# Performance work log

Measured on AMD Instinct MI355X. Metric: run time of the kernel, lower is better.

Reference implementation:

```python
import jax, jax.numpy as jnp
import numpy as np

DIM = 384; HEADS = 6; POINTS = 4; LEVELS = 3; HID = 96
B = 2; D0 = 12; H0 = 12; W0 = 12
NMID = D0 * H0 * W0          # mid-level tokens
NTOK = 73 * NMID // 8        # total tokens across 3 scales


def _ln(x, w, b, eps=1e-6):
    m = x.mean(-1, keepdims=True)
    v = ((x - m) ** 2).mean(-1, keepdims=True)
    return (x - m) * jax.lax.rsqrt(v + eps) * w + b


def _make_ref(shapes):
    # matches get_reference_points: per-level normalized centers, stacked as (d, x, y)
    refs = []
    for (D_, H_, W_) in shapes:
        d = (jnp.arange(D_, dtype=jnp.float32) + 0.5) / D_
        y = (jnp.arange(H_, dtype=jnp.float32) + 0.5) / H_
        x = (jnp.arange(W_, dtype=jnp.float32) + 0.5) / W_
        dd, yy, xx = jnp.meshgrid(d, y, x, indexing='ij')
        refs.append(jnp.stack([dd.ravel(), xx.ravel(), yy.ravel()], -1))
    return jnp.concatenate(refs, 0)[None, :, None, :]  # [1, N, 1, 3]


def _sample_level(v, D_, H_, W_, loc):
    # v: [B,S,h,hd]; loc: [B,Nq,h,P,3] normalized (d,x,y); trilinear, zero padding,
    # align_corners=False semantics (pixel = norm*size - 0.5)
    Bq, Nq, h, P, _ = loc.shape
    hd = v.shape[-1]
    pd = loc[..., 0] * D_ - 0.5
    px = loc[..., 1] * W_ - 0.5
    py = loc[..., 2] * H_ - 0.5
    d0 = jnp.floor(pd); x0 = jnp.floor(px); y0 = jnp.floor(py)
    fd = pd - d0; fx = px - x0; fy = py - y0
    d0 = d0.astype(jnp.int32); x0 = x0.astype(jnp.int32); y0 = y0.astype(jnp.int32)
    acc = jnp.zeros((Bq, Nq, h, P, hd), v.dtype)
    for dd in (0, 1):  # fixed 8-corner loop
        for dy in (0, 1):
            for dx in (0, 1):
                di = d0 + dd; yi = y0 + dy; xi = x0 + dx
                wgt = (fd if dd else 1.0 - fd) * (fy if dy else 1.0 - fy) * (fx if dx else 1.0 - fx)
                valid = ((di >= 0) & (di < D_) & (yi >= 0) & (yi < H_) & (xi >= 0) & (xi < W_)).astype(v.dtype)
                idx = (jnp.clip(di, 0, D_ - 1) * H_ + jnp.clip(yi, 0, H_ - 1)) * W_ + jnp.clip(xi, 0, W_ - 1)
                idx_t = idx.transpose(0, 1, 3, 2).reshape(Bq, Nq * P, h)
                g = jnp.take_along_axis(v, idx_t[..., None], axis=1)  # [B,Nq*P,h,hd]
                g = g.reshape(Bq, Nq, P, h, hd).transpose(0, 1, 3, 2, 4)
                acc = acc + (wgt * valid)[..., None] * g
    return acc  # [B,Nq,h,P,hd]


def _msdeform(q, ref, feat, shapes, off_w, off_b, aw_w, aw_b, val_w, val_b, out_w, out_b):
    Bq, Nq, C = q.shape
    hd = C // HEADS
    value = (feat @ val_w + val_b).reshape(Bq, -1, HEADS, hd)
    off = (q @ off_w + off_b).reshape(Bq, Nq, HEADS, LEVELS, POINTS, 3)
    aw = jax.nn.softmax((q @ aw_w + aw_b).reshape(Bq, Nq, HEADS, LEVELS * POINTS), -1)
    aw = aw.reshape(Bq, Nq, HEADS, LEVELS, POINTS)
    # offset normalizer in (d, x, y) order -> (D, W, H)
    norm = jnp.array([[D_, W_, H_] for (D_, H_, W_) in shapes], dtype=q.dtype)
    loc = ref[:, :, None, :, None, :] + off / norm[None, None, None, :, None, :]
    out = jnp.zeros((Bq, Nq, HEADS, hd), q.dtype)
    start = 0
    for l, (D_, H_, W_) in enumerate(shapes):
        S = D_ * H_ * W_
        sampled = _sample_level(value[:, start:start + S], D_, H_, W_, loc[:, :, :, l])
        out = out + jnp.einsum('bqhp,bqhpd->bqhd', aw[:, :, :, l], sampled)
        start += S
    return out.reshape(Bq, Nq, C) @ out_w + out_b


def _dwconv_seg(x, Dv, Hv, Wv, w, b):
    Bq, S, C = x.shape
    xv = x.reshape(Bq, Dv, Hv, Wv, C)
    y = jax.lax.conv_general_dilated(xv, w, (1, 1, 1), 'SAME',
                                     dimension_numbers=('NDHWC', 'DHWIO', 'NDHWC'),
                                     feature_group_count=C) + b
    return y.reshape(Bq, S, C)


def _conv_ffn(x, D, H, W, fc1_w, fc1_b, dw_w, dw_b, fc2_w, fc2_b):
    x = x @ fc1_w + fc1_b
    n = x.shape[1] // 73
    x1 = _dwconv_seg(x[:, :64 * n], 2 * D, 2 * H, 2 * W, dw_w, dw_b)
    x2 = _dwconv_seg(x[:, 64 * n:72 * n], D, H, W, dw_w, dw_b)
    x3 = _dwconv_seg(x[:, 72 * n:], D // 2, H // 2, W // 2, dw_w, dw_b)
    x = jax.nn.gelu(jnp.concatenate([x1, x2, x3], 1), approximate=False)
    return x @ fc2_w + fc2_b


def _forward(query, feat, D, H, W,
             qnorm_w, qnorm_b, fnorm_w, fnorm_b, ext_qnorm_w, ext_qnorm_b,
             ext_fnorm_w, ext_fnorm_b, ffn_norm_w, ffn_norm_b,
             off_w, off_b, aw_w, aw_b, val_w, val_b, out_w, out_b,
             fc1_w, fc1_b, dw_w, dw_b, fc2_w, fc2_b):
    n_mid = D * H * W
    n_high = 8 * n_mid
    x2 = query[:, n_high:n_high + n_mid] + feat
    q = jnp.concatenate([query[:, :n_high], x2, query[:, n_high + n_mid:]], 1)
    shapes = [(2 * D, 2 * H, 2 * W), (D, H, W), (D // 2, H // 2, W // 2)]
    ref = _make_ref(shapes)
    qn = _ln(q, qnorm_w, qnorm_b)      # CTI_toC.query_norm
    fn = _ln(q, fnorm_w, fnorm_b)      # CTI_toC.feat_norm
    aq = _ln(qn, ext_qnorm_w, ext_qnorm_b)  # MultiscaleExtractor.query_norm
    af = _ln(fn, ext_fnorm_w, ext_fnorm_b)  # MultiscaleExtractor.feat_norm
    out = qn + _msdeform(aq, ref, af, shapes, off_w, off_b, aw_w, aw_b, val_w, val_b, out_w, out_b)
    out = out + _conv_ffn(_ln(out, ffn_norm_w, ffn_norm_b), D, H, W,
                          fc1_w, fc1_b, dw_w, dw_b, fc2_w, fc2_b)
    return out


def setup_inputs() -> dict:
    key = jax.random.key(0)
    ks = jax.random.split(key, 16)
    w = lambda k, *s: jax.random.normal(k, s, jnp.float32) * 0.02
    NO = HEADS * LEVELS * POINTS * 3
    NA = HEADS * LEVELS * POINTS
    return {
        'query': jax.random.normal(ks[0], (B, NTOK, DIM), jnp.float32),
        'reference_points': jax.random.uniform(ks[1], (1, NTOK, 1, 3), dtype=jnp.float32),
        'feat': jax.random.normal(ks[2], (B, NMID, DIM), jnp.float32),
        'spatial_shapes': jnp.array([[2 * D0, 2 * H0, 2 * W0], [D0, H0, W0], [D0 // 2, H0 // 2, W0 // 2]], jnp.int32),
        'level_start_index': jnp.array([0, 8 * NMID, 9 * NMID], jnp.int32),
        'D': D0, 'H': H0, 'W': W0,
        'qnorm_w': jnp.ones(DIM), 'qnorm_b': jnp.zeros(DIM),
        'fnorm_w': jnp.ones(DIM), 'fnorm_b': jnp.zeros(DIM),
        'ext_qnorm_w': jnp.ones(DIM), 'ext_qnorm_b': jnp.zeros(DIM),
        'ext_fnorm_w': jnp.ones(DIM), 'ext_fnorm_b': jnp.zeros(DIM),
        'ffn_norm_w': jnp.ones(DIM), 'ffn_norm_b': jnp.zeros(DIM),
        'off_w': w(ks[3], DIM, NO), 'off_b': jnp.zeros(NO),
        'aw_w': w(ks[4], DIM, NA), 'aw_b': jnp.zeros(NA),
        'val_w': w(ks[5], DIM, DIM), 'val_b': jnp.zeros(DIM),
        'out_w': w(ks[6], DIM, DIM), 'out_b': jnp.zeros(DIM),
        'fc1_w': w(ks[7], DIM, HID), 'fc1_b': jnp.zeros(HID),
        'dw_w': w(ks[8], 3, 3, 3, 1, HID), 'dw_b': jnp.zeros(HID),
        'fc2_w': w(ks[9], HID, DIM), 'fc2_b': jnp.zeros(DIM),
    }


def reference(query, reference_points, feat, spatial_shapes, level_start_index, D, H, W,
              qnorm_w, qnorm_b, fnorm_w, fnorm_b, ext_qnorm_w, ext_qnorm_b,
              ext_fnorm_w, ext_fnorm_b, ffn_norm_w, ffn_norm_b,
              off_w, off_b, aw_w, aw_b, val_w, val_b, out_w, out_b,
              fc1_w, fc1_b, dw_w, dw_b, fc2_w, fc2_b):
    # reference_points / spatial_shapes / level_start_index are required by the torch
    # signature but unused: CTI_toC recomputes deform inputs internally.
    return _forward(query, feat, D, H, W,
                    qnorm_w, qnorm_b, fnorm_w, fnorm_b, ext_qnorm_w, ext_qnorm_b,
                    ext_fnorm_w, ext_fnorm_b, ffn_norm_w, ffn_norm_b,
                    off_w, off_b, aw_w, aw_b, val_w, val_b, out_w, out_b,
                    fc1_w, fc1_b, dw_w, dw_b, fc2_w, fc2_b)
```

## Files before the change

### kernel.cpp

```cpp
#include <hip/hip_runtime.h>
#include <hip/hip_fp16.h>
#include <cstdint>
#include <cstddef>

#define DIM    384
#define HEADS  6
#define HD     64
#define NTOK   15768
#define NMID   1728
#define BATCH  2
#define ROWS   (BATCH*NTOK)
#define MPAD   31616
#define L1START 13824
#define L2START 15552
#define HID    96
#define VROWS  (ROWS + 8)
#define VSLAB  ((size_t)VROWS * 64)

typedef __attribute__((ext_vector_type(8))) short short8;
typedef __attribute__((ext_vector_type(4))) float floatx4;

__device__ __forceinline__ unsigned short f2bf(float x){
  unsigned u = __float_as_uint(x);
  unsigned r = (u + 0x7FFFu + ((u >> 16) & 1u)) >> 16;
  return (unsigned short)r;
}

__device__ __forceinline__ unsigned cvt_pk_bf16(float lo, float hi){
  unsigned r;
  asm("v_cvt_pk_bf16_f32 %0, %1, %2" : "=v"(r) : "v"(lo), "v"(hi));
  return r;
}

__device__ __forceinline__ float wave_sum(float v){
  #pragma unroll
  for (int o = 32; o; o >>= 1) v += __shfl_xor(v, o, 64);
  return v;
}

__device__ __forceinline__ void ln384(const float* x, float* y,
                                      const float* __restrict__ w,
                                      const float* __restrict__ b, int lane){
  float s = 0.f;
  #pragma unroll
  for (int j = 0; j < 6; j++) s += x[j];
  s = wave_sum(s);
  float m = s * (1.f/384.f);
  float v = 0.f;
  #pragma unroll
  for (int j = 0; j < 6; j++){ float d = x[j] - m; v += d*d; }
  v = wave_sum(v) * (1.f/384.f);
  float rs = rsqrtf(v + 1e-6f);
  #pragma unroll
  for (int j = 0; j < 6; j++){
    int c = j*64 + lane;
    y[j] = (x[j] - m) * rs * w[c] + b[c];
  }
}

__global__ void k_ln_front(const float* __restrict__ query, const float* __restrict__ feat,
                           const float* __restrict__ qw,  const float* __restrict__ qb,
                           const float* __restrict__ fw,  const float* __restrict__ fb,
                           const float* __restrict__ eqw, const float* __restrict__ eqb,
                           const float* __restrict__ efw, const float* __restrict__ efb,
                           float* __restrict__ qn, unsigned short* __restrict__ aq,
                           unsigned short* __restrict__ af){
  int wid = blockIdx.x * (blockDim.x >> 6) + (threadIdx.x >> 6);
  if (wid >= ROWS) return;
  int lane = threadIdx.x & 63;
  int b = wid / NTOK, t = wid - b*NTOK;
  const float* qp = query + (size_t)wid * DIM;
  float x[6];
  #pragma unroll
  for (int j = 0; j < 6; j++) x[j] = qp[j*64 + lane];
  if (t >= L1START && t < L2START){
    const float* fp = feat + ((size_t)b*NMID + (t - L1START)) * DIM;
    #pragma unroll
    for (int j = 0; j < 6; j++) x[j] += fp[j*64 + lane];
  }
  float y[6], z[6];
  ln384(x, y, qw, qb, lane);
  {
    float* o = qn + (size_t)wid * DIM;
    #pragma unroll
    for (int j = 0; j < 6; j++) o[j*64 + lane] = y[j];
  }
  ln384(y, z, eqw, eqb, lane);
  {
    unsigned short* o = aq + (size_t)wid * DIM;
    #pragma unroll
    for (int j = 0; j < 6; j++) o[j*64 + lane] = f2bf(z[j]);
  }
  ln384(x, y, fw, fb, lane);
  ln384(y, z, efw, efb, lane);
  {
    unsigned short* o = af + (size_t)wid * DIM;
    #pragma unroll
    for (int j = 0; j < 6; j++) o[j*64 + lane] = f2bf(z[j]);
  }
}

__global__ void k_ln(const float* __restrict__ in, const float* __restrict__ w,
                     const float* __restrict__ b, unsigned short* __restrict__ out){
  int wid = blockIdx.x * (blockDim.x >> 6) + (threadIdx.x >> 6);
  if (wid >= ROWS) return;
  int lane = threadIdx.x & 63;
  float x[6], y[6];
  const float* p = in + (size_t)wid * DIM;
  #pragma unroll
  for (int j = 0; j < 6; j++) x[j] = p[j*64 + lane];
  ln384(x, y, w, b, lane);
  unsigned short* o = out + (size_t)wid * DIM;
  #pragma unroll
  for (int j = 0; j < 6; j++) o[j*64 + lane] = f2bf(y[j]);
}

__global__ void k_cvt_all(const float* __restrict__ val_w, const float* __restrict__ off_w,
                          const float* __restrict__ aw_w,  const float* __restrict__ out_w,
                          const float* __restrict__ fc1_w, const float* __restrict__ fc2_w,
                          const float* __restrict__ off_b, const float* __restrict__ aw_b,
                          unsigned short* __restrict__ wt_val, unsigned short* __restrict__ wt_offaw,
                          unsigned short* __restrict__ wt_out, unsigned short* __restrict__ wt_fc1,
                          unsigned short* __restrict__ wt_fc2, float* __restrict__ offaw_b,
                          unsigned short* __restrict__ vt_pad){
  int id = blockIdx.x * blockDim.x + threadIdx.x;
  if (id < 147456){
    int n = id / 384, k = id - n*384;
    wt_val[id] = f2bf(val_w[(size_t)k*384 + n]);
  } else if (id < 294912){
    int i = id - 147456;
    int n = i / 384, k = i - n*384;
    float v = 0.f;
    if (n < 216) v = off_w[(size_t)k*216 + n];
    else if (n >= 256 && n < 328) v = aw_w[(size_t)k*72 + (n-256)];
    wt_offaw[i] = f2bf(v);
  } else if (id < 442368){
    int i = id - 294912;
    int n = i / 384, k = i - n*384;
    wt_out[i] = f2bf(out_w[(size_t)k*384 + n]);
  } else if (id < 491520){
    int i = id - 442368;
    int n = i / 384, k = i - n*384;
    wt_fc1[i] = f2bf((n < 96) ? fc1_w[(size_t)k*96 + n] : 0.f);
  } else if (id < 528384){
    int i = id - 491520;
    int n = i / 96, k = i - n*96;
    wt_fc2[i] = f2bf(fc2_w[(size_t)k*384 + n]);
  } else if (id < 528768){
    int n = id - 528384;
    float v = 0.f;
    if (n < 216) v = off_b[n];
    else if (n >= 256 && n < 328) v = aw_b[n-256];
    offaw_b[n] = v;
  } else if (id < 531840){
    int i = id - 528768;
    int hh = i >> 9, rem = i & 511;
    vt_pad[(size_t)hh * VSLAB + (size_t)ROWS * 64 + rem] = 0;
  }
}

template<int OUTMODE>
__global__ __launch_bounds__(256) void k_gemm(
    const unsigned short* __restrict__ A,
    const unsigned short* __restrict__ Wt,
    const float* __restrict__ bias,
    const float* __restrict__ R,
    void* __restrict__ Cv,
    int M, int N, int K){
  __shared__ __align__(16) unsigned short As[128*32];
  __shared__ __align__(16) unsigned short Bs[128*32];
  int tid = threadIdx.x;
  int w = tid >> 6, lane = tid & 63;
  int m0 = blockIdx.y * 128, n0 = blockIdx.x * 128;
  int m_off = (w & 1) * 64, n_off = (w >> 1) * 64;

  floatx4 acc[4][4] = {};

  int sr = lane >> 2;
  int sc = (lane & 3) * 8;
  int lrow = lane & 15;
  int kq = (lane >> 4) * 8;

  for (int k0 = 0; k0 < K; k0 += 32){
    #pragma unroll
    for (int s = 0; s < 2; s++){
      int c = w * 2 + s;
      const unsigned short* ga = A  + (size_t)(m0 + c*16 + sr) * K + k0 + sc;
      __builtin_amdgcn_global_load_lds(
          (const __attribute__((address_space(1))) void*)ga,
          (__attribute__((address_space(3))) void*)(As + c*512), 16, 0, 0);
      const unsigned short* gb = Wt + (size_t)(n0 + c*16 + sr) * K + k0 + sc;
      __builtin_amdgcn_global_load_lds(
          (const __attribute__((address_space(1))) void*)gb,
          (__attribute__((address_space(3))) void*)(Bs + c*512), 16, 0, 0);
    }
    __syncthreads();
    short8 afr[4], bfr[4];
    #pragma unroll
    for (int i = 0; i < 4; i++)
      afr[i] = *(const short8*)(As + (m_off + i*16 + lrow)*32 + kq);
    #pragma unroll
    for (int j = 0; j < 4; j++)
      bfr[j] = *(const short8*)(Bs + (n_off + j*16 + lrow)*32 + kq);
    #pragma unroll
    for (int i = 0; i < 4; i++)
      #pragma unroll
      for (int j = 0; j < 4; j++)
        acc[i][j] = __builtin_amdgcn_mfma_f32_16x16x32_bf16(afr[i], bfr[j], acc[i][j], 0, 0, 0);
    __syncthreads();
  }

  int cn = n0 + n_off + lrow;
  int rbase = m0 + m_off + (lane >> 4) * 4;
  #pragma unroll
  for (int j = 0; j < 4; j++){
    int n = cn + j*16;
    if (n >= N) continue;
    float bj = bias[n];
    #pragma unroll
    for (int i = 0; i < 4; i++){
      int mb = rbase + i*16;
      #pragma unroll
      for (int r = 0; r < 4; r++){
        int m = mb + r;
        if (m < M){
          float v = acc[i][j][r] + bj;
          if (R) v += R[(size_t)m * N + n];
          if (OUTMODE == 0)      ((float*)Cv)[(size_t)m * N + n] = v;
          else if (OUTMODE == 1) ((unsigned short*)Cv)[(size_t)m * N + n] = f2bf(v);
          else {
            ((__half*)Cv)[(size_t)(n >> 6) * VSLAB + (size_t)m * 64 + (n & 63)] =
                __float2half_rn(v);
          }
        }
      }
    }
  }
}

__global__ __launch_bounds__(64, 4) void k_msdeform(const __half* __restrict__ vt,
                                                    const float* __restrict__ offaw,
                                                    unsigned short* __restrict__ msout){
  int head = blockIdx.x;
  int r    = blockIdx.y;
  int lane = threadIdx.x & 63;
  int b = (r >= NTOK) ? 1 : 0;
  int t = r - b * NTOK;

  float refd, refy, refx;
  if (t < L1START){
    int i = t;
    int dd = i / 576; int rem = i - dd*576; int yy = rem / 24; int xx = rem - yy*24;
    refd = (dd + 0.5f) * (1.f/24.f); refy = (yy + 0.5f) * (1.f/24.f); refx = (xx + 0.5f) * (1.f/24.f);
  } else if (t < L2START){
    int i = t - L1START;
    int dd = i / 144; int rem = i - dd*144; int yy = rem / 12; int xx = rem - yy*12;
    refd = (dd + 0.5f) * (1.f/12.f); refy = (yy + 0.5f) * (1.f/12.f); refx = (xx + 0.5f) * (1.f/12.f);
  } else {
    int i = t - L2START;
    int dd = i / 36; int rem = i - dd*36; int yy = rem / 6; int xx = rem - yy*6;
    refd = (dd + 0.5f) * (1.f/6.f); refy = (yy + 0.5f) * (1.f/6.f); refx = (xx + 0.5f) * (1.f/6.f);
  }

  int s   = lane & 15;
  int grp = lane >> 4;

  float logit = (s < 12) ? offaw[(size_t)r * 384 + 256 + head * 12 + s] : -1e30f;
  float mx = logit;
  mx = fmaxf(mx, __shfl_xor(mx, 1, 64));
  mx = fmaxf(mx, __shfl_xor(mx, 2, 64));
  mx = fmaxf(mx, __shfl_xor(mx, 4, 64));
  mx = fmaxf(mx, __shfl_xor(mx, 8, 64));
  float e = (s < 12) ? __expf(logit - mx) : 0.f;
  float sum = e;
  sum += __shfl_xor(sum, 1, 64);
  sum += __shfl_xor(sum, 2, 64);
  sum += __shfl_xor(sum, 4, 64);
  sum += __shfl_xor(sum, 8, 64);
  float aww = e / sum;

  int rowk = 0, wgtk = 0;
  if (s < 12){
    int j = s;
    int l = j >> 2;
    int Dl  = (l == 0) ? 24 : ((l == 1) ? 12 : 6);
    int lst = (l == 0) ? 0  : ((l == 1) ? L1START : L2START);
    const float* op = offaw + (size_t)r * 384 + head * 36 + j * 3;
    float od = op[0], ox = op[1], oy = op[2];
    float fDl = (float)Dl;
    float pd = refd * fDl + od - 0.5f;
    float px = refx * fDl + ox - 0.5f;
    float py = refy * fDl + oy - 0.5f;
    float fld = floorf(pd), flx = floorf(px), fly = floorf(py);
    float fd = pd - fld, fx = px - flx, fy = py - fly;
    int d0 = (int)fld, x0 = (int)flx, y0 = (int)fly;
    int cz = grp >> 1, cy = grp & 1;
    int di = d0 + cz, yi = y0 + cy;
    bool vzy = (di >= 0) & (di < Dl) & (yi >= 0) & (yi < Dl);
    float wz = cz ? fd : 1.f - fd;
    float wy = cy ? fy : 1.f - fy;
    float wp = vzy ? (wz * aww) * wy : 0.f;
    int rs = min(max(x0, 0), Dl - 1);
    float wlo_x = (rs == x0) ? (1.f - fx) : ((rs == x0 + 1) ? fx : 0.f);
    float whi_x = ((rs == x0) && (x0 + 1 < Dl)) ? fx : 0.f;
    int dc = min(max(di, 0), Dl - 1);
    int yc = min(max(yi, 0), Dl - 1);
    rowk = (b * NTOK + lst) + (dc * Dl + yc) * Dl + rs;
    __half2 wh = __floats2half2_rn(wp * wlo_x, wp * whi_x);
    wgtk = *(int*)&wh;
  }

  const char* vbase = (const char*)(vt + (size_t)head * VSLAB);
  unsigned laneoff = (unsigned)(lane & 15) << 4;
  unsigned selperm = (lane & 8) ? 0x03020302u : 0x01000100u;

  uint4 vd[12]; unsigned wv[12];
  #define MS_LOAD(J) { int rw_ = __builtin_amdgcn_ds_swizzle(rowk, ((J) << 5) | 16); \
    vd[J] = *(const uint4*)(vbase + ((((unsigned)rw_) << 7) + laneoff)); }
  MS_LOAD(0)  MS_LOAD(1)  MS_LOAD(2)  MS_LOAD(3)
  MS_LOAD(4)  MS_LOAD(5)  MS_LOAD(6)  MS_LOAD(7)
  MS_LOAD(8)  MS_LOAD(9)  MS_LOAD(10) MS_LOAD(11)
  #undef MS_LOAD
  #define MS_W(J) { unsigned wj_ = (unsigned)__builtin_amdgcn_ds_swizzle(wgtk, ((J) << 5) | 16); \
    wv[J] = __builtin_amdgcn_perm(wj_, wj_, selperm); }
  MS_W(0)  MS_W(1)  MS_W(2)  MS_W(3)
  MS_W(4)  MS_W(5)  MS_W(6)  MS_W(7)
  MS_W(8)  MS_W(9)  MS_W(10) MS_W(11)
  #undef MS_W

  __half2 hz; *(int*)&hz = 0;
  __half2 a0 = hz, a1 = hz, a2 = hz, a3 = hz;
  #pragma unroll
  for (int j = 0; j < 12; j++){
    __half2 wh = *(__half2*)&wv[j];
    uint4 v = vd[j];
    a0 = __hfma2(wh, *(__half2*)&v.x, a0);
    a1 = __hfma2(wh, *(__half2*)&v.y, a1);
    a2 = __hfma2(wh, *(__half2*)&v.z, a2);
    a3 = __hfma2(wh, *(__half2*)&v.w, a3);
  }

  int i0 = *(int*)&a0, i1 = *(int*)&a1, i2 = *(int*)&a2, i3 = *(int*)&a3;
  int p0 = __shfl_xor(i0, 8, 64); int p1 = __shfl_xor(i1, 8, 64);
  int p2 = __shfl_xor(i2, 8, 64); int p3 = __shfl_xor(i3, 8, 64);
  a0 = __hadd2(a0, *(__half2*)&p0);
  a1 = __hadd2(a1, *(__half2*)&p1);
  a2 = __hadd2(a2, *(__half2*)&p2);
  a3 = __hadd2(a3, *(__half2*)&p3);
  float2 f0 = __half22float2(a0), f1 = __half22float2(a1);
  float2 f2 = __half22float2(a2), f3 = __half22float2(a3);
  float sv[8] = {f0.x, f0.y, f1.x, f1.y, f2.x, f2.y, f3.x, f3.y};
  #pragma unroll
  for (int k = 0; k < 8; k++){
    sv[k] += __shfl_xor(sv[k], 16, 64);
    sv[k] += __shfl_xor(sv[k], 32, 64);
  }

  if (lane < 8){
    uint4 pk;
    pk.x = cvt_pk_bf16(sv[0], sv[1]);
    pk.y = cvt_pk_bf16(sv[2], sv[3]);
    pk.z = cvt_pk_bf16(sv[4], sv[5]);
    pk.w = cvt_pk_bf16(sv[6], sv[7]);
    *(uint4*)(msout + (size_t)r * DIM + head * 64 + lane * 8) = pk;
  }
}

__global__ void k_dwconv_gelu(const float* __restrict__ h, const float* __restrict__ dww,
                              const float* __restrict__ dwb, unsigned short* __restrict__ h2){
  int gid = blockIdx.x * blockDim.x + threadIdx.x;
  if (gid >= ROWS * 24) return;
  int c4 = gid % 24;
  int r = gid / 24;
  int c = c4 * 4;
  int b = (r >= NTOK) ? 1 : 0;
  int t = r - b * NTOK;
  int base, DL, i;
  if (t < L1START){ base = 0; DL = 24; i = t; }
  else if (t < L2START){ base = L1START; DL = 12; i = t - L1START; }
  else { base = L2START; DL = 6; i = t - L2START; }
  int dd, yy, xx;
  if (DL == 24){ dd = i / 576; int rem = i - dd*576; yy = rem / 24; xx = rem - yy*24; }
  else if (DL == 12){ dd = i / 144; int rem = i - dd*144; yy = rem / 12; xx = rem - yy*12; }
  else { dd = i / 36; int rem = i - dd*36; yy = rem / 6; xx = rem - yy*6; }
  float4 acc = {0.f, 0.f, 0.f, 0.f};
  #pragma unroll
  for (int kz = 0; kz < 3; kz++){
    int nd = dd + kz - 1; if (nd < 0 || nd >= DL) continue;
    #pragma unroll
    for (int ky = 0; ky < 3; ky++){
      int ny = yy + ky - 1; if (ny < 0 || ny >= DL) continue;
      #pragma unroll
      for (int kx = 0; kx < 3; kx++){
        int nx = xx + kx - 1; if (nx < 0 || nx >= DL) continue;
        int nt = base + (nd * DL + ny) * DL + nx;
        float4 hv = *(const float4*)(h + ((size_t)(b*NTOK + nt)) * HID + c);
        float4 wv = *(const float4*)(dww + (size_t)((kz*3 + ky)*3 + kx) * HID + c);
        acc.x += hv.x * wv.x; acc.y += hv.y * wv.y;
        acc.z += hv.z * wv.z; acc.w += hv.w * wv.w;
      }
    }
  }
  float4 bv = *(const float4*)(dwb + c);
  acc.x += bv.x; acc.y += bv.y; acc.z += bv.z; acc.w += bv.w;
  const float k = 0.70710678118654752440f;
  float g0 = 0.5f * acc.x * (1.f + erff(acc.x * k));
  float g1 = 0.5f * acc.y * (1.f + erff(acc.y * k));
  float g2 = 0.5f * acc.z * (1.f + erff(acc.z * k));
  float g3 = 0.5f * acc.w * (1.f + erff(acc.w * k));
  uint2 pk;
  pk.x = ((unsigned)f2bf(g1) << 16) | (unsigned)f2bf(g0);
  pk.y = ((unsigned)f2bf(g3) << 16) | (unsigned)f2bf(g2);
  *(uint2*)(h2 + (size_t)r * HID + c) = pk;
}

extern "C" void kernel_launch(void* const* d_in, const int* in_sizes, int n_in,
                              void* d_out, int out_size, void* d_ws, size_t ws_size,
                              hipStream_t stream){
  const float* query = (const float*)d_in[0];
  const float* feat  = (const float*)d_in[2];
  const float* qnw = (const float*)d_in[8],  *qnb = (const float*)d_in[9];
  const float* fnw = (const float*)d_in[10], *fnb = (const float*)d_in[11];
  const float* eqw = (const float*)d_in[12], *eqb = (const float*)d_in[13];
  const float* efw = (const float*)d_in[14], *efb = (const float*)d_in[15];
  const float* ffw = (const float*)d_in[16], *ffb = (const float*)d_in[17];
  const float* off_w = (const float*)d_in[18], *off_b = (const float*)d_in[19];
  const float* aw_w  = (const float*)d_in[20], *aw_b  = (const float*)d_in[21];
  const float* val_w = (const float*)d_in[22], *val_b = (const float*)d_in[23];
  const float* out_w = (const float*)d_in[24], *out_b = (const float*)d_in[25];
  const float* fc1_w = (const float*)d_in[26], *fc1_b = (const float*)d_in[27];
  const float* dw_w  = (const float*)d_in[28], *dw_b  = (const float*)d_in[29];
  const float* fc2_w = (const float*)d_in[30], *fc2_b = (const float*)d_in[31];
  float* out = (float*)d_out;

  char* p = (char*)d_ws;
  float* qn             = (float*)p;          p += (size_t)ROWS*384*4;
  unsigned short* aq    = (unsigned short*)p; p += (size_t)MPAD*384*2;
  unsigned short* af    = (unsigned short*)p; p += (size_t)MPAD*384*2;
  __half* value_t       = (__half*)p;         p += (size_t)HEADS*VSLAB*2;
  float* offaw          = (float*)p;          p += (size_t)ROWS*384*4;
  unsigned short* wt_val   = (unsigned short*)p; p += (size_t)384*384*2;
  unsigned short* wt_offaw = (unsigned short*)p; p += (size_t)384*384*2;
  unsigned short* wt_out   = (unsigned short*)p; p += (size_t)384*384*2;
  unsigned short* wt_fc1   = (unsigned short*)p; p += (size_t)128*384*2;
  unsigned short* wt_fc2   = (unsigned short*)p; p += (size_t)384*96*2;
  float* offaw_b           = (float*)p;          p += (size_t)384*4;
  unsigned short* t_buf  = aq;
  unsigned short* msout  = af;
  float* y1              = offaw;
  float* h_buf           = (float*)value_t;
  unsigned short* h2_buf = (unsigned short*)qn;

  k_cvt_all<<<(531840 + 255)/256, 256, 0, stream>>>(val_w, off_w, aw_w, out_w, fc1_w, fc2_w,
                                                    off_b, aw_b,
                                                    wt_val, wt_offaw, wt_out, wt_fc1, wt_fc2,
                                                    offaw_b, (unsigned short*)value_t);

  int lnBlocks = ROWS / 4;
  k_ln_front<<<lnBlocks, 256, 0, stream>>>(query, feat, qnw, qnb, fnw, fnb,
                                           eqw, eqb, efw, efb, qn, aq, af);

  dim3 gN384(3, MPAD/128), gN128(1, MPAD/128);

  k_gemm<2><<<gN384, 256, 0, stream>>>(af, wt_val, val_b, nullptr, value_t, ROWS, 384, 384);
  k_gemm<0><<<gN384, 256, 0, stream>>>(aq, wt_offaw, offaw_b, nullptr, offaw, ROWS, 384, 384);
  k_msdeform<<<dim3(HEADS, ROWS), 64, 0, stream>>>(value_t, offaw, msout);
  k_gemm<0><<<gN384, 256, 0, stream>>>(msout, wt_out, out_b, qn, y1, ROWS, 384, 384);
  k_ln<<<lnBlocks, 256, 0, stream>>>(y1, ffw, ffb, t_buf);
  k_gemm<0><<<gN128, 256, 0, stream>>>(t_buf, wt_fc1, fc1_b, nullptr, h_buf, ROWS, 96, 384);
  k_dwconv_gelu<<<(ROWS * 24 + 255)/256, 256, 0, stream>>>(h_buf, dw_w, dw_b, h2_buf);
  k_gemm<0><<<gN384, 256, 0, stream>>>(h2_buf, wt_fc2, fc2_b, y1, out, ROWS, 384, 96);
}
```

Baseline: 488.0 us.

## Double-buffer GEMM LDS tiles and restructure msdeform reductions and block order

The GEMM kernel now double-buffers its A/B LDS tiles, prefetching the next K-slice with global_load_lds while MFMAs run on the current one. This removes one barrier per iteration and hides load latency, at the cost of twice the shared memory. The msdeform kernel now uses a 1D grid with a block remap that groups blocks by head, and passes sampling descriptors through LDS instead of ds_swizzle. Its softmax and output reductions use DPP and permlane32_swap on packed half2 values instead of float shuffles, which adds some fp16 rounding risk in the final sums.

```diff
diff --git a/kernel.cpp b/kernel.cpp
--- a/kernel.cpp
+++ b/kernel.cpp
@@ -30,6 +30,28 @@
   unsigned r;
   asm("v_cvt_pk_bf16_f32 %0, %1, %2" : "=v"(r) : "v"(lo), "v"(hi));
   return r;
+}
+
+template<int C>
+__device__ __forceinline__ int dpp_i(int v){
+  return __builtin_amdgcn_mov_dpp(v, C, 0xF, 0xF, true);
+}
+template<int C>
+__device__ __forceinline__ float dpp_f(float v){
+  return __int_as_float(dpp_i<C>(__float_as_int(v)));
+}
+#define ROR8 0x128
+#define ROR4 0x124
+#define ROR2 0x122
+#define ROR1 0x121
+
+__device__ __forceinline__ __half2 h2_of(int v){ return *(__half2*)&v; }
+__device__ __forceinline__ int i_of(__half2 v){ return *(int*)&v; }
+
+__device__ __forceinline__ __half2 xor32_hadd(__half2 a){
+  int x = i_of(a), y = x;
+  asm volatile("v_permlane32_swap_b32 %0, %1" : "+v"(x), "+v"(y));
+  return __hadd2(h2_of(x), h2_of(y));
 }
 
 __device__ __forceinline__ float wave_sum(float v){
@@ -167,8 +189,8 @@
     const float* __restrict__ R,
     void* __restrict__ Cv,
     int M, int N, int K){
-  __shared__ __align__(16) unsigned short As[128*32];
-  __shared__ __align__(16) unsigned short Bs[128*32];
+  __shared__ __align__(16) unsigned short As[2*128*32];
+  __shared__ __align__(16) unsigned short Bs[2*128*32];
   int tid = threadIdx.x;
   int w = tid >> 6, lane = tid & 63;
   int m0 = blockIdx.y * 128, n0 = blockIdx.x * 128;
@@ -181,34 +203,44 @@
   int lrow = lane & 15;
   int kq = (lane >> 4) * 8;
 
+#define GSTAGE(BUF, K0) { \
+    _Pragma("unroll") \
+    for (int s2 = 0; s2 < 2; s2++){ \
+      int c = w * 2 + s2; \
+      const unsigned short* ga = A  + (size_t)(m0 + c*16 + sr) * K + (K0) + sc; \
+      __builtin_amdgcn_global_load_lds( \
+          (const __attribute__((address_space(1))) void*)ga, \
+          (__attribute__((address_space(3))) void*)(As + (BUF)*4096 + c*512), 16, 0, 0); \
+      const unsigned short* gb = Wt + (size_t)(n0 + c*16 + sr) * K + (K0) + sc; \
+      __builtin_amdgcn_global_load_lds( \
+          (const __attribute__((address_space(1))) void*)gb, \
+          (__attribute__((address_space(3))) void*)(Bs + (BUF)*4096 + c*512), 16, 0, 0); \
+    } }
+
+  GSTAGE(0, 0)
+  __syncthreads();
+
+  int cur = 0;
   for (int k0 = 0; k0 < K; k0 += 32){
-    #pragma unroll
-    for (int s = 0; s < 2; s++){
-      int c = w * 2 + s;
-      const unsigned short* ga = A  + (size_t)(m0 + c*16 + sr) * K + k0 + sc;
-      __builtin_amdgcn_global_load_lds(
-          (const __attribute__((address_space(1))) void*)ga,
-          (__attribute__((address_space(3))) void*)(As + c*512), 16, 0, 0);
-      const unsigned short* gb = Wt + (size_t)(n0 + c*16 + sr) * K + k0 + sc;
-      __builtin_amdgcn_global_load_lds(
-          (const __attribute__((address_space(1))) void*)gb,
-          (__attribute__((address_space(3))) void*)(Bs + c*512), 16, 0, 0);
-    }
-    __syncthreads();
+    if (k0 + 32 < K){ GSTAGE(cur ^ 1, k0 + 32) }
+    const unsigned short* Ab = As + cur*4096;
+    const unsigned short* Bb = Bs + cur*4096;
     short8 afr[4], bfr[4];
     #pragma unroll
     for (int i = 0; i < 4; i++)
-      afr[i] = *(const short8*)(As + (m_off + i*16 + lrow)*32 + kq);
+      afr[i] = *(const short8*)(Ab + (m_off + i*16 + lrow)*32 + kq);
     #pragma unroll
     for (int j = 0; j < 4; j++)
-      bfr[j] = *(const short8*)(Bs + (n_off + j*16 + lrow)*32 + kq);
+      bfr[j] = *(const short8*)(Bb + (n_off + j*16 + lrow)*32 + kq);
     #pragma unroll
     for (int i = 0; i < 4; i++)
       #pragma unroll
       for (int j = 0; j < 4; j++)
         acc[i][j] = __builtin_amdgcn_mfma_f32_16x16x32_bf16(afr[i], bfr[j], acc[i][j], 0, 0, 0);
     __syncthreads();
-  }
+    cur ^= 1;
+  }
+#undef GSTAGE
 
   int cn = n0 + n_off + lrow;
   int rbase = m0 + m_off + (lane >> 4) * 4;
@@ -241,8 +273,11 @@
 __global__ __launch_bounds__(64, 4) void k_msdeform(const __half* __restrict__ vt,
                                                     const float* __restrict__ offaw,
                                                     unsigned short* __restrict__ msout){
-  int head = blockIdx.x;
-  int r    = blockIdx.y;
+  __shared__ __align__(16) int2 dsc[48];
+  int bid = blockIdx.x;
+  int seq = (bid & 7) * ((ROWS*HEADS)/8) + (bid >> 3);
+  int head = seq / ROWS;
+  int r = seq - head * ROWS;
   int lane = threadIdx.x & 63;
   int b = (r >= NTOK) ? 1 : 0;
   int t = r - b * NTOK;
@@ -267,19 +302,18 @@
 
   float logit = (s < 12) ? offaw[(size_t)r * 384 + 256 + head * 12 + s] : -1e30f;
   float mx = logit;
-  mx = fmaxf(mx, __shfl_xor(mx, 1, 64));
-  mx = fmaxf(mx, __shfl_xor(mx, 2, 64));
-  mx = fmaxf(mx, __shfl_xor(mx, 4, 64));
-  mx = fmaxf(mx, __shfl_xor(mx, 8, 64));
+  mx = fmaxf(mx, dpp_f<ROR8>(mx));
+  mx = fmaxf(mx, dpp_f<ROR4>(mx));
+  mx = fmaxf(mx, dpp_f<ROR2>(mx));
+  mx = fmaxf(mx, dpp_f<ROR1>(mx));
   float e = (s < 12) ? __expf(logit - mx) : 0.f;
   float sum = e;
-  sum += __shfl_xor(sum, 1, 64);
-  sum += __shfl_xor(sum, 2, 64);
-  sum += __shfl_xor(sum, 4, 64);
-  sum += __shfl_xor(sum, 8, 64);
+  sum += dpp_f<ROR8>(sum);
+  sum += dpp_f<ROR4>(sum);
+  sum += dpp_f<ROR2>(sum);
+  sum += dpp_f<ROR1>(sum);
   float aww = e / sum;
 
-  int rowk = 0, wgtk = 0;
   if (s < 12){
     int j = s;
     int l = j >> 2;
@@ -305,34 +339,37 @@
     float whi_x = ((rs == x0) && (x0 + 1 < Dl)) ? fx : 0.f;
     int dc = min(max(di, 0), Dl - 1);
     int yc = min(max(yi, 0), Dl - 1);
-    rowk = (b * NTOK + lst) + (dc * Dl + yc) * Dl + rs;
+    int rowk = (b * NTOK + lst) + (dc * Dl + yc) * Dl + rs;
     __half2 wh = __floats2half2_rn(wp * wlo_x, wp * whi_x);
-    wgtk = *(int*)&wh;
-  }
+    dsc[grp * 12 + s] = make_int2(rowk, *(int*)&wh);
+  }
+  const uint4* dq = (const uint4*)dsc;
+  uint4 dp0 = dq[grp*6+0], dp1 = dq[grp*6+1], dp2 = dq[grp*6+2];
+  uint4 dp3 = dq[grp*6+3], dp4 = dq[grp*6+4], dp5 = dq[grp*6+5];
 
   const char* vbase = (const char*)(vt + (size_t)head * VSLAB);
   unsigned laneoff = (unsigned)(lane & 15) << 4;
   unsigned selperm = (lane & 8) ? 0x03020302u : 0x01000100u;
 
-  uint4 vd[12]; unsigned wv[12];
-  #define MS_LOAD(J) { int rw_ = __builtin_amdgcn_ds_swizzle(rowk, ((J) << 5) | 16); \
-    vd[J] = *(const uint4*)(vbase + ((((unsigned)rw_) << 7) + laneoff)); }
-  MS_LOAD(0)  MS_LOAD(1)  MS_LOAD(2)  MS_LOAD(3)
-  MS_LOAD(4)  MS_LOAD(5)  MS_LOAD(6)  MS_LOAD(7)
-  MS_LOAD(8)  MS_LOAD(9)  MS_LOAD(10) MS_LOAD(11)
-  #undef MS_LOAD
-  #define MS_W(J) { unsigned wj_ = (unsigned)__builtin_amdgcn_ds_swizzle(wgtk, ((J) << 5) | 16); \
-    wv[J] = __builtin_amdgcn_perm(wj_, wj_, selperm); }
-  MS_W(0)  MS_W(1)  MS_W(2)  MS_W(3)
-  MS_W(4)  MS_W(5)  MS_W(6)  MS_W(7)
-  MS_W(8)  MS_W(9)  MS_W(10) MS_W(11)
-  #undef MS_W
+  int rw[12] = {(int)dp0.x,(int)dp0.z,(int)dp1.x,(int)dp1.z,(int)dp2.x,(int)dp2.z,
+                (int)dp3.x,(int)dp3.z,(int)dp4.x,(int)dp4.z,(int)dp5.x,(int)dp5.z};
+  unsigned wg[12] = {dp0.y,dp0.w,dp1.y,dp1.w,dp2.y,dp2.w,
+                     dp3.y,dp3.w,dp4.y,dp4.w,dp5.y,dp5.w};
+
+  uint4 vd[12];
+  #pragma unroll
+  for (int j = 0; j < 12; j++)
+    vd[j] = *(const uint4*)(vbase + ((((unsigned)rw[j]) << 7) + laneoff));
+  unsigned wsel[12];
+  #pragma unroll
+  for (int j = 0; j < 12; j++)
+    wsel[j] = __builtin_amdgcn_perm(wg[j], wg[j], selperm);
 
   __half2 hz; *(int*)&hz = 0;
   __half2 a0 = hz, a1 = hz, a2 = hz, a3 = hz;
   #pragma unroll
   for (int j = 0; j < 12; j++){
-    __half2 wh = *(__half2*)&wv[j];
+    __half2 wh = *(__half2*)&wsel[j];
     uint4 v = vd[j];
     a0 = __hfma2(wh, *(__half2*)&v.x, a0);
     a1 = __hfma2(wh, *(__half2*)&v.y, a1);
@@ -340,28 +377,29 @@
     a3 = __hfma2(wh, *(__half2*)&v.w, a3);
   }
 
-  int i0 = *(int*)&a0, i1 = *(int*)&a1, i2 = *(int*)&a2, i3 = *(int*)&a3;
-  int p0 = __shfl_xor(i0, 8, 64); int p1 = __shfl_xor(i1, 8, 64);
-  int p2 = __shfl_xor(i2, 8, 64); int p3 = __shfl_xor(i3, 8, 64);
-  a0 = __hadd2(a0, *(__half2*)&p0);
-  a1 = __hadd2(a1, *(__half2*)&p1);
-  a2 = __hadd2(a2, *(__half2*)&p2);
-  a3 = __hadd2(a3, *(__half2*)&p3);
-  float2 f0 = __half22float2(a0), f1 = __half22float2(a1);
-  float2 f2 = __half22float2(a2), f3 = __half22float2(a3);
-  float sv[8] = {f0.x, f0.y, f1.x, f1.y, f2.x, f2.y, f3.x, f3.y};
-  #pragma unroll
-  for (int k = 0; k < 8; k++){
-    sv[k] += __shfl_xor(sv[k], 16, 64);
-    sv[k] += __shfl_xor(sv[k], 32, 64);
-  }
+  a0 = __hadd2(a0, h2_of(dpp_i<ROR8>(i_of(a0))));
+  a1 = __hadd2(a1, h2_of(dpp_i<ROR8>(i_of(a1))));
+  a2 = __hadd2(a2, h2_of(dpp_i<ROR8>(i_of(a2))));
+  a3 = __hadd2(a3, h2_of(dpp_i<ROR8>(i_of(a3))));
+  {
+    int t0 = __shfl_xor(i_of(a0), 16, 64); a0 = __hadd2(a0, h2_of(t0));
+    int t1 = __shfl_xor(i_of(a1), 16, 64); a1 = __hadd2(a1, h2_of(t1));
+    int t2 = __shfl_xor(i_of(a2), 16, 64); a2 = __hadd2(a2, h2_of(t2));
+    int t3 = __shfl_xor(i_of(a3), 16, 64); a3 = __hadd2(a3, h2_of(t3));
+  }
+  a0 = xor32_hadd(a0);
+  a1 = xor32_hadd(a1);
+  a2 = xor32_hadd(a2);
+  a3 = xor32_hadd(a3);
 
   if (lane < 8){
+    float2 f0 = __half22float2(a0), f1 = __half22float2(a1);
+    float2 f2 = __half22float2(a2), f3 = __half22float2(a3);
     uint4 pk;
-    pk.x = cvt_pk_bf16(sv[0], sv[1]);
-    pk.y = cvt_pk_bf16(sv[2], sv[3]);
-    pk.z = cvt_pk_bf16(sv[4], sv[5]);
-    pk.w = cvt_pk_bf16(sv[6], sv[7]);
+    pk.x = cvt_pk_bf16(f0.x, f0.y);
+    pk.y = cvt_pk_bf16(f1.x, f1.y);
+    pk.z = cvt_pk_bf16(f2.x, f2.y);
+    pk.w = cvt_pk_bf16(f3.x, f3.y);
     *(uint4*)(msout + (size_t)r * DIM + head * 64 + lane * 8) = pk;
   }
 }
@@ -464,7 +502,7 @@
 
   k_gemm<2><<<gN384, 256, 0, stream>>>(af, wt_val, val_b, nullptr, value_t, ROWS, 384, 384);
   k_gemm<0><<<gN384, 256, 0, stream>>>(aq, wt_offaw, offaw_b, nullptr, offaw, ROWS, 384, 384);
-  k_msdeform<<<dim3(HEADS, ROWS), 64, 0, stream>>>(value_t, offaw, msout);
+  k_msdeform<<<ROWS * HEADS, 64, 0, stream>>>(value_t, offaw, msout);
   k_gemm<0><<<gN384, 256, 0, stream>>>(msout, wt_out, out_b, qn, y1, ROWS, 384, 384);
   k_ln<<<lnBlocks, 256, 0, stream>>>(y1, ffw, ffb, t_buf);
   k_gemm<0><<<gN128, 256, 0, stream>>>(t_buf, wt_fc1, fc1_b, nullptr, h_buf, ROWS, 96, 384);
```

New measurement: 472.5 us. 3.2% less time.
